# Performance work log

Measured on AMD Instinct MI355X. Metric: run time of the kernel, lower is better.

## Reference

```python
import jax, jax.numpy as jnp
import numpy as np

PAD = 32  # integer padding from init_kwargs

def _conv1d_fft(x, weight, bias):
    # x: (B, Cin, L), weight: (Cout, Cin, K), bias: (Cout,)
    B, Cin, L = x.shape
    Cout, _, K = weight.shape
    p = PAD
    padded = (L + 2 * p + 31) & ~31          # round up to multiple of 32
    out_len = 2 * p + L - (K - 1)
    offset = (min(K, L) - 1) // 2 - p
    roll = -((K - 1) // 2) + offset
    # pad kernel to padded length then circularly roll (centers the kernel)
    k_pad = jnp.pad(weight, ((0, 0), (0, 0), (0, padded - K)))
    k_rolled = jnp.roll(k_pad, roll, axis=-1)
    x_fft = jnp.fft.rfft(x, n=padded, axis=-1)          # (B, Cin, F)
    k_fft = jnp.fft.rfft(k_rolled, axis=-1)             # (Cout, Cin, F)
    # multiply-reduce over in_channels == batched complex GEMM over freq bins
    b_fft = jnp.einsum('bif,oif->bof', x_fft, jnp.conj(k_fft))
    # bias enters only the DC bin, scaled by padded length (irfft normalization)
    b_fft = b_fft.at[..., 0].add(bias.astype(b_fft.dtype) * padded)
    b = jnp.fft.irfft(b_fft, n=padded, axis=-1)
    return b[..., :out_len]


def setup_inputs() -> dict:
    key = jax.random.key(0)
    k1, k2, k3 = jax.random.split(key, 3)
    B, Cin, Cout, L, K = 16, 128, 128, 4096, 129
    stdv = 1.0 / np.sqrt(Cin * K)
    x = jax.random.normal(k1, (B, Cin, L), dtype=jnp.float32)
    weight = jax.random.uniform(k2, (Cout, Cin, K), dtype=jnp.float32, minval=-stdv, maxval=stdv)
    bias = jax.random.uniform(k3, (Cout,), dtype=jnp.float32, minval=-stdv, maxval=stdv)
    return {"x": x, "weight": weight, "bias": bias}


def reference(x, weight, bias):
    return _conv1d_fft(x, weight, bias)
```

## Files before the change

### kernel.cpp

```cpp
#include <hip/hip_runtime.h>


typedef _Float16 f16;
typedef _Float16 f16x8 __attribute__((ext_vector_type(8)));
typedef float f32x4 __attribute__((ext_vector_type(4)));

#define NB   16
#define CI   128
#define CO   128
#define LIN  4096
#define KW   129
#define TOUT 4032
#define UPAD 4224
#define XT_BYTES ((size_t)NB * 2 * 8 * UPAD * 16)
#define WLDS 32768

__device__ __forceinline__ void gld16(void* lds, const void* g) {
    __builtin_amdgcn_global_load_lds(
        (const __attribute__((address_space(1))) unsigned int*)g,
        (__attribute__((address_space(3))) unsigned int*)lds,
        16, 0, 0);
}

__global__ __launch_bounds__(256) void xt_prep(const float* __restrict__ x,
                                               f16* __restrict__ xt) {
    __shared__ float tile[128][33];
    const int b  = blockIdx.y;
    const int u0 = blockIdx.x * 32;
    const int l0 = u0 - 32;
    const int tid = threadIdx.x;
    const int col = tid & 31;
    const int cib = tid >> 5;
#pragma unroll
    for (int r = 0; r < 16; ++r) {
        int ci = cib + r * 8;
        int l  = l0 + col;
        float v = 0.f;
        if (l >= 0 && l < LIN) v = x[((size_t)b * CI + ci) * LIN + l];
        tile[ci][col] = v;
    }
    __syncthreads();
#pragma unroll
    for (int it = 0; it < 2; ++it) {
        int idx   = tid + it * 256;
        int chunk = idx >> 5;
        int ur    = idx & 31;
        f16x8 v;
#pragma unroll
        for (int j = 0; j < 8; ++j) v[j] = (f16)tile[chunk * 8 + j][ur];
        size_t unit = ((size_t)b * 16 + chunk) * UPAD + (u0 + ur);
        *(f16x8*)(&xt[unit * 8]) = v;
    }
}

__global__ __launch_bounds__(256) void wt_prep(const float* __restrict__ w,
                                               f16* __restrict__ wt) {
    __shared__ float tile[32][132];
    const int cic = blockIdx.x;
    const int co  = blockIdx.y;
    const int ci0 = cic * 32;
    const int tid = threadIdx.x;
    for (int it = 0; it < 17; ++it) {
        int idx = tid + it * 256;
        if (idx < 32 * 129) {
            int i = idx / 129;
            int m = idx - i * 129;
            tile[i][m] = w[(size_t)co * (CI * KW) + (size_t)(ci0 + i) * KW + m];
        }
    }
    __syncthreads();
    for (int it = 0; it < 3; ++it) {
        int idx = tid + it * 256;
        if (idx < 129 * 4) {
            int m = idx >> 2;
            int c = idx & 3;
            int kk = m * 4 + cic;
            f16x8 v;
#pragma unroll
            for (int j = 0; j < 8; ++j) v[j] = (f16)tile[c * 8 + j][m];
            *(f16x8*)(&wt[(size_t)kk * 4096 + c * 1024 + co * 8]) = v;
        }
    }
}

__global__ __launch_bounds__(256, 2) void conv_main(
    const f16* __restrict__ xt, const f16* __restrict__ wt,
    const float* __restrict__ bias, float* __restrict__ out)
{
    extern __shared__ char smem[];
    const int tid  = threadIdx.x;
    const int lane = tid & 63;
    const int wid  = tid >> 6;
    const int l15  = lane & 15;
    const int l4   = lane >> 4;
    const int wco  = (wid >> 1) << 6;
    const int wtt  = (wid & 1) << 6;

    const int tt = blockIdx.x;
    const int b  = blockIdx.y;
    const int u0 = tt << 7;

    const char* wbase = (const char*)wt;
    char* wring = smem + WLDS;

    int aoff[4];
#pragma unroll
    for (int ct = 0; ct < 4; ++ct)
        aoff[ct] = l4 * 2048 + (wco + ct * 16 + l15) * 16;
    int qb[2];
#pragma unroll
    for (int q = 0; q < 2; ++q) qb[q] = (q * 4 + l4) * 4096;
    int xoff[4];
#pragma unroll
    for (int st = 0; st < 4; ++st)
        xoff[st] = (wtt + st * 16 + l15) * 16;

    f32x4 acc[4][4];
#pragma unroll
    for (int i = 0; i < 4; ++i)
#pragma unroll
        for (int j = 0; j < 4; ++j)
            acc[i][j] = (f32x4){0.f, 0.f, 0.f, 0.f};

    f16x8 afA[2][4], bfA[2][4], afB[2][4], bfB[2][4];

    for (int p = 0; p < 2; ++p) {
        const int pbase = 2 * p;

        if (p) {
            asm volatile("s_waitcnt lgkmcnt(0)" ::: "memory");
            __builtin_amdgcn_s_barrier();
        }
        const char* xph = (const char*)xt +
            (((size_t)b * 16 + p * 8) * UPAD + u0) * 16;
#pragma unroll
        for (int i = 0; i < 8; ++i)
            gld16(smem + tid * 16 + i * 4096, xph + (size_t)i * (UPAD * 16) + tid * 16);
        {
            const char* ws0 = wbase + (size_t)pbase * 8192;
            gld16(wring + tid * 16,         ws0 + tid * 16);
            gld16(wring + 4096 + tid * 16,  ws0 + 4096 + tid * 16);
            gld16(wring + 8192 + tid * 16,  ws0 + 8192 + tid * 16);
            gld16(wring + 12288 + tid * 16, ws0 + 12288 + tid * 16);
            const char* ws1 = wbase + (size_t)(4 + pbase) * 8192;
            gld16(wring + 16384 + tid * 16, ws1 + tid * 16);
            gld16(wring + 20480 + tid * 16, ws1 + 4096 + tid * 16);
            gld16(wring + 24576 + tid * 16, ws1 + 8192 + tid * 16);
            gld16(wring + 28672 + tid * 16, ws1 + 12288 + tid * 16);
        }
        asm volatile("s_waitcnt vmcnt(4)" ::: "memory");
        __builtin_amdgcn_s_barrier();
        __builtin_amdgcn_sched_barrier(0);

#pragma unroll
        for (int q = 0; q < 2; ++q) {
#pragma unroll
            for (int ct = 0; ct < 4; ++ct)
                afA[q][ct] = *(const f16x8*)(wring + q * 8192 + aoff[ct]);
#pragma unroll
            for (int st = 0; st < 4; ++st)
                bfA[q][st] = *(const f16x8*)(smem + qb[q] + xoff[st]);
        }

        int rpF = 1, rpD = 2;

        auto body = [&](int t, f16x8 (&afC)[2][4], f16x8 (&bfC)[2][4],
                               f16x8 (&afN)[2][4], f16x8 (&bfN)[2][4]) {
            const bool issue = (t + 2 <= 128);
            if (issue) {
                const char* wsrc = wbase + (size_t)(4 * (t + 2) + pbase) * 8192;
                char* dst = wring + rpD * 16384;
                gld16(dst + tid * 16,         wsrc + tid * 16);
                gld16(dst + 4096 + tid * 16,  wsrc + 4096 + tid * 16);
                gld16(dst + 8192 + tid * 16,  wsrc + 8192 + tid * 16);
                gld16(dst + 12288 + tid * 16, wsrc + 12288 + tid * 16);
                asm volatile("s_waitcnt vmcnt(4)" ::: "memory");
            } else {
                asm volatile("s_waitcnt vmcnt(0)" ::: "memory");
            }
            __builtin_amdgcn_s_barrier();
            __builtin_amdgcn_sched_barrier(0);
            if (t + 1 <= 128) {
                const int mn = (t + 1) * 16;
                const char* wl = wring + rpF * 16384;
#pragma unroll
                for (int q = 0; q < 2; ++q) {
#pragma unroll
                    for (int ct = 0; ct < 4; ++ct)
                        afN[q][ct] = *(const f16x8*)(wl + q * 8192 + aoff[ct]);
#pragma unroll
                    for (int st = 0; st < 4; ++st)
                        bfN[q][st] = *(const f16x8*)(smem + qb[q] + xoff[st] + mn);
                }
            }
#pragma unroll
            for (int q = 0; q < 2; ++q)
#pragma unroll
                for (int ct = 0; ct < 4; ++ct)
#pragma unroll
                    for (int st = 0; st < 4; ++st)
                        acc[ct][st] = __builtin_amdgcn_mfma_f32_16x16x32_f16(
                            afC[q][ct], bfC[q][st], acc[ct][st], 0, 0, 0);
            rpF = (rpF == 2) ? 0 : rpF + 1;
            rpD = (rpD == 2) ? 0 : rpD + 1;
        };

        for (int t2 = 0; t2 < 128; t2 += 2) {
            body(t2,     afA, bfA, afB, bfB);
            body(t2 + 1, afB, bfB, afA, bfA);
        }
        body(128, afA, bfA, afB, bfB);
    }

#pragma unroll
    for (int ct = 0; ct < 4; ++ct) {
#pragma unroll
        for (int r = 0; r < 4; ++r) {
            int co = wco + ct * 16 + l4 * 4 + r;
            float bv = bias[co];
            float* orow = out + ((size_t)b * CO + co) * TOUT;
#pragma unroll
            for (int st = 0; st < 4; ++st) {
                int t = u0 + wtt + st * 16 + l15;
                if (t < TOUT) orow[t] = acc[ct][st][r] + bv;
            }
        }
    }
}

extern "C" void kernel_launch(void* const* d_in, const int* in_sizes, int n_in,
                              void* d_out, int out_size, void* d_ws, size_t ws_size,
                              hipStream_t stream) {
    const float* x    = (const float*)d_in[0];
    const float* w    = (const float*)d_in[1];
    const float* bias = (const float*)d_in[2];
    float* out = (float*)d_out;

    f16* xt = (f16*)d_ws;
    f16* wt = (f16*)((char*)d_ws + XT_BYTES);

    xt_prep<<<dim3(UPAD / 32, NB), 256, 0, stream>>>(x, xt);
    wt_prep<<<dim3(4, CO), 256, 0, stream>>>(w, wt);
    conv_main<<<dim3(32, NB), 256, 81920, stream>>>(xt, wt, bias, out);
}
```

Before: 310.2 us.

## Load weight fragments directly from global memory instead of LDS ring buffer

Removes the triple-buffered LDS ring for weights, along with its per-step async global-to-LDS copies, waitcnt and barrier. Each wave now reads its weight MFMA fragments straight from global memory into registers, one step ahead. LDS use drops from 80KB to 32KB, which could raise occupancy. The cost is exposed global or L2 latency on the weight loads, which are now only one step ahead, and redundant weight reads across waves.

```diff
diff --git a/kernel.cpp b/kernel.cpp
--- a/kernel.cpp
+++ b/kernel.cpp
@@ -13,7 +13,6 @@
 #define TOUT 4032
 #define UPAD 4224
 #define XT_BYTES ((size_t)NB * 2 * 8 * UPAD * 16)
-#define WLDS 32768
 
 __device__ __forceinline__ void gld16(void* lds, const void* g) {
     __builtin_amdgcn_global_load_lds(
@@ -101,19 +100,8 @@
     const int u0 = tt << 7;
 
     const char* wbase = (const char*)wt;
-    char* wring = smem + WLDS;
-
-    int aoff[4];
-#pragma unroll
-    for (int ct = 0; ct < 4; ++ct)
-        aoff[ct] = l4 * 2048 + (wco + ct * 16 + l15) * 16;
-    int qb[2];
-#pragma unroll
-    for (int q = 0; q < 2; ++q) qb[q] = (q * 4 + l4) * 4096;
-    int xoff[4];
-#pragma unroll
-    for (int st = 0; st < 4; ++st)
-        xoff[st] = (wtt + st * 16 + l15) * 16;
+    const int alane = l4 * 2048 + wco * 16 + l15 * 16;
+    const int blane = l4 * 4096 + (wtt + l15) * 16;
 
     f32x4 acc[4][4];
 #pragma unroll
@@ -136,62 +124,41 @@
 #pragma unroll
         for (int i = 0; i < 8; ++i)
             gld16(smem + tid * 16 + i * 4096, xph + (size_t)i * (UPAD * 16) + tid * 16);
+
         {
-            const char* ws0 = wbase + (size_t)pbase * 8192;
-            gld16(wring + tid * 16,         ws0 + tid * 16);
-            gld16(wring + 4096 + tid * 16,  ws0 + 4096 + tid * 16);
-            gld16(wring + 8192 + tid * 16,  ws0 + 8192 + tid * 16);
-            gld16(wring + 12288 + tid * 16, ws0 + 12288 + tid * 16);
-            const char* ws1 = wbase + (size_t)(4 + pbase) * 8192;
-            gld16(wring + 16384 + tid * 16, ws1 + tid * 16);
-            gld16(wring + 20480 + tid * 16, ws1 + 4096 + tid * 16);
-            gld16(wring + 24576 + tid * 16, ws1 + 8192 + tid * 16);
-            gld16(wring + 28672 + tid * 16, ws1 + 12288 + tid * 16);
-        }
-        asm volatile("s_waitcnt vmcnt(4)" ::: "memory");
+            const char* a0 = wbase + (size_t)pbase * 8192 + alane;
+#pragma unroll
+            for (int q = 0; q < 2; ++q)
+#pragma unroll
+                for (int ct = 0; ct < 4; ++ct)
+                    afA[q][ct] = *(const f16x8*)(a0 + q * 8192 + ct * 256);
+        }
+        asm volatile("s_waitcnt vmcnt(0)" ::: "memory");
         __builtin_amdgcn_s_barrier();
-        __builtin_amdgcn_sched_barrier(0);
-
-#pragma unroll
-        for (int q = 0; q < 2; ++q) {
-#pragma unroll
-            for (int ct = 0; ct < 4; ++ct)
-                afA[q][ct] = *(const f16x8*)(wring + q * 8192 + aoff[ct]);
+
+#pragma unroll
+        for (int q = 0; q < 2; ++q)
 #pragma unroll
             for (int st = 0; st < 4; ++st)
-                bfA[q][st] = *(const f16x8*)(smem + qb[q] + xoff[st]);
-        }
-
-        int rpF = 1, rpD = 2;
+                bfA[q][st] = *(const f16x8*)(smem + blane + q * 16384 + st * 256);
 
         auto body = [&](int t, f16x8 (&afC)[2][4], f16x8 (&bfC)[2][4],
                                f16x8 (&afN)[2][4], f16x8 (&bfN)[2][4]) {
-            const bool issue = (t + 2 <= 128);
-            if (issue) {
-                const char* wsrc = wbase + (size_t)(4 * (t + 2) + pbase) * 8192;
-                char* dst = wring + rpD * 16384;
-                gld16(dst + tid * 16,         wsrc + tid * 16);
-                gld16(dst + 4096 + tid * 16,  wsrc + 4096 + tid * 16);
-                gld16(dst + 8192 + tid * 16,  wsrc + 8192 + tid * 16);
-                gld16(dst + 12288 + tid * 16, wsrc + 12288 + tid * 16);
-                asm volatile("s_waitcnt vmcnt(4)" ::: "memory");
-            } else {
-                asm volatile("s_waitcnt vmcnt(0)" ::: "memory");
-            }
             __builtin_amdgcn_s_barrier();
-            __builtin_amdgcn_sched_barrier(0);
             if (t + 1 <= 128) {
-                const int mn = (t + 1) * 16;
-                const char* wl = wring + rpF * 16384;
-#pragma unroll
-                for (int q = 0; q < 2; ++q) {
+                const int tn = t + 1;
+                const char* an = wbase + (size_t)(4 * tn + pbase) * 8192 + alane;
+                const char* bn = smem + blane + tn * 16;
+#pragma unroll
+                for (int q = 0; q < 2; ++q)
 #pragma unroll
                     for (int ct = 0; ct < 4; ++ct)
-                        afN[q][ct] = *(const f16x8*)(wl + q * 8192 + aoff[ct]);
+                        afN[q][ct] = *(const f16x8*)(an + q * 8192 + ct * 256);
+#pragma unroll
+                for (int q = 0; q < 2; ++q)
 #pragma unroll
                     for (int st = 0; st < 4; ++st)
-                        bfN[q][st] = *(const f16x8*)(smem + qb[q] + xoff[st] + mn);
-                }
+                        bfN[q][st] = *(const f16x8*)(bn + q * 16384 + st * 256);
             }
 #pragma unroll
             for (int q = 0; q < 2; ++q)
@@ -201,8 +168,6 @@
                     for (int st = 0; st < 4; ++st)
                         acc[ct][st] = __builtin_amdgcn_mfma_f32_16x16x32_f16(
                             afC[q][ct], bfC[q][st], acc[ct][st], 0, 0, 0);
-            rpF = (rpF == 2) ? 0 : rpF + 1;
-            rpD = (rpD == 2) ? 0 : rpD + 1;
         };
 
         for (int t2 = 0; t2 < 128; t2 += 2) {
@@ -241,5 +206,5 @@
 
     xt_prep<<<dim3(UPAD / 32, NB), 256, 0, stream>>>(x, xt);
     wt_prep<<<dim3(4, CO), 256, 0, stream>>>(w, wt);
-    conv_main<<<dim3(32, NB), 256, 81920, stream>>>(xt, wt, bias, out);
-}
+    conv_main<<<dim3(32, NB), 256, 32768, stream>>>(xt, wt, bias, out);
+}
```

Result: slower. 343.3 us (+10.7%).
